# Kernel optimization log

Hardware: AMD Instinct MI355X
Metric: run time of the kernel (lower is better)

The kernel has to match this reference:

```python
import jax, jax.numpy as jnp
import numpy as np

ALPHA = 0.25
GAMMA = 2.0
EPS = 1e-4


def calc_iou(a, b):
    # a: [A,4] anchors xyxy, b: [M,4] gt boxes xyxy -> [A,M]
    area = (b[:, 2] - b[:, 0]) * (b[:, 3] - b[:, 1])  # [M]
    iw = jnp.minimum(a[:, 2:3], b[None, :, 2]) - jnp.maximum(a[:, 0:1], b[None, :, 0])
    ih = jnp.minimum(a[:, 3:4], b[None, :, 3]) - jnp.maximum(a[:, 1:2], b[None, :, 1])
    iw = jnp.clip(iw, 0.0)
    ih = jnp.clip(ih, 0.0)
    anchor_area = ((a[:, 2] - a[:, 0]) * (a[:, 3] - a[:, 1]))[:, None]
    ua = jnp.clip(anchor_area + area[None, :] - iw * ih, 1e-8)
    return iw * ih / ua


def setup_inputs() -> dict:
    B, A, K, M = 8, 120000, 80, 32
    key = jax.random.key(0)
    k1, k2, k3, k4, k5, k6, k7 = jax.random.split(key, 7)
    classifications = jax.random.uniform(k1, (B, A, K), dtype=jnp.float32)
    regressions = jax.random.normal(k2, (B, A, 4), dtype=jnp.float32) * 0.1
    # anchors: valid xyxy boxes with positive width/height
    a_xy = jax.random.uniform(k3, (A, 2), minval=0.0, maxval=480.0)
    a_wh = jax.random.uniform(k4, (A, 2), minval=16.0, maxval=128.0)
    anchors = jnp.concatenate([a_xy, a_xy + a_wh], axis=1)[None].astype(jnp.float32)
    # annotations: [B, M, 5] valid gt boxes, labels in [0, K)
    g_xy = jax.random.uniform(k5, (B, M, 2), minval=0.0, maxval=400.0)
    g_wh = jax.random.uniform(k6, (B, M, 2), minval=20.0, maxval=120.0)
    labels = jax.random.randint(k7, (B, M, 1), 0, K).astype(jnp.float32)
    annotations = jnp.concatenate([g_xy, g_xy + g_wh, labels], axis=2).astype(jnp.float32)
    return {"classifications": classifications, "regressions": regressions,
            "anchors": anchors, "annotations": annotations}


def reference(classifications, regressions, anchors, annotations):
    anchor = anchors[0]  # [A,4]
    aw = anchor[:, 2] - anchor[:, 0]
    ah = anchor[:, 3] - anchor[:, 1]
    acx = anchor[:, 0] + 0.5 * aw
    acy = anchor[:, 1] + 0.5 * ah
    reg_scale = jnp.array([0.1, 0.1, 0.2, 0.2], dtype=classifications.dtype)

    def per_item(cls, reg, ann):
        # cls: [A,K], reg: [A,4], ann: [M,5]
        valid = ann[:, 4] != -1.0  # [M] padding mask
        c = jnp.clip(cls, EPS, 1.0 - EPS)
        iou = jnp.where(valid[None, :], calc_iou(anchor, ann[:, :4]), -1.0)  # [A,M]
        iou_max = iou.max(axis=1)
        iou_argmax = iou.argmax(axis=1)
        assigned = ann[iou_argmax]  # [A,5] gather
        pos = iou_max >= 0.5
        neg = iou_max < 0.4
        num_pos = pos.sum().astype(c.dtype)
        # targets: 1 at assigned class for positives, 0 for negatives, -1 = ignore
        onehot = jax.nn.one_hot(assigned[:, 4].astype(jnp.int32), c.shape[1], dtype=c.dtype)
        t = jnp.where(pos[:, None], onehot, jnp.where(neg[:, None], 0.0, -1.0))
        alpha_factor = jnp.where(t == 1.0, ALPHA, 1.0 - ALPHA)
        focal_weight = jnp.where(t == 1.0, 1.0 - c, c)
        bce = -(t * jnp.log(c) + (1.0 - t) * jnp.log(1.0 - c))
        cls_loss = jnp.where(t != -1.0, alpha_factor * focal_weight ** GAMMA * bce, 0.0)
        cls_loss = cls_loss.sum() / jnp.maximum(num_pos, 1.0)
        gw0 = assigned[:, 2] - assigned[:, 0]
        gh0 = assigned[:, 3] - assigned[:, 1]
        gcx = assigned[:, 0] + 0.5 * gw0
        gcy = assigned[:, 1] + 0.5 * gh0
        gw = jnp.maximum(gw0, 1.0)
        gh = jnp.maximum(gh0, 1.0)
        rt = jnp.stack([(gcx - acx) / aw, (gcy - acy) / ah,
                        jnp.log(gw / aw), jnp.log(gh / ah)], axis=1) / reg_scale
        diff = jnp.abs(rt - reg)
        smooth = jnp.where(diff <= 1.0 / 9.0, 0.5 * 9.0 * diff ** 2, diff - 0.5 / 9.0)
        reg_loss = jnp.where(num_pos > 0.0,
                             (smooth * pos[:, None]).sum() / jnp.maximum(num_pos * 4.0, 1.0),
                             0.0)
        return cls_loss, reg_loss

    cls_l, reg_l = jax.vmap(per_item)(classifications, regressions, annotations)
    return cls_l.mean(keepdims=True), reg_l.mean(keepdims=True)
```

## Files before the change

kernel.cpp:

```cpp
#include <hip/hip_runtime.h>

#define NB 8
#define NA 120000
#define NK 80
#define NM 32

#define ALPHA_F 0.25f
#define EPS_F 1e-4f

#define TPB (NA / 64)
#define BLKW 4
#define BPBW ((TPB + BLKW - 1) / BLKW)


typedef float f32x4 __attribute__((ext_vector_type(4)));

__device__ __forceinline__ f32x4 ntload4(const f32x4* p) {
    return __builtin_nontemporal_load(p);
}

__device__ __forceinline__ float clampc(float x) {
    return fminf(fmaxf(x, EPS_F), 1.0f - EPS_F);
}
__device__ __forceinline__ float negl(float c) {
    return (1.0f - ALPHA_F) * c * c * (-__logf(1.0f - c));
}
__device__ __forceinline__ float posl(float c) {
    const float omc = 1.0f - c;
    return ALPHA_F * omc * omc * (-__logf(c));
}
__device__ __forceinline__ float negl4v(f32x4 v) {
    return negl(clampc(v.x)) + negl(clampc(v.y)) + negl(clampc(v.z)) + negl(clampc(v.w));
}

__global__ __launch_bounds__(256) void fused_kernel(
    const float* __restrict__ anchors,
    const float* __restrict__ regressions,
    const float* __restrict__ annotations,
    const float* __restrict__ cls,
    float* __restrict__ part)
{
    const int b = blockIdx.x / BPBW;
    const int blk = blockIdx.x % BPBW;
    const int wid = threadIdx.x >> 6;
    const int lane = threadIdx.x & 63;
    const int tile = blk * BLKW + wid;

    __shared__ float ann[NM * 5];
    __shared__ float barea[NM];
    if (threadIdx.x < NM * 5) ann[threadIdx.x] = annotations[b * NM * 5 + threadIdx.x];
    __syncthreads();
    if (threadIdx.x < NM) {
        const float* r = &ann[threadIdx.x * 5];
        barea[threadIdx.x] = (r[2] - r[0]) * (r[3] - r[1]);
    }
    __syncthreads();

    float reg_local = 0.0f;
    float pos_local = 0.0f;
    float cls_local = 0.0f;

    if (tile < TPB) {
        const int a = tile * 64 + lane;
        float maskf = 1.0f;

        {
            const float4 av = ((const float4*)anchors)[a];
            const float aw = av.z - av.x;
            const float ah = av.w - av.y;
            const float aarea = aw * ah;

            float bi = -1.0f, bu = 1.0f;
            int bm = 0;
            #pragma unroll
            for (int m = 0; m < NM; ++m) {
                const float bx1 = ann[m * 5 + 0];
                const float by1 = ann[m * 5 + 1];
                const float bx2 = ann[m * 5 + 2];
                const float by2 = ann[m * 5 + 3];
                const float lbl = ann[m * 5 + 4];
                const float iw = fmaxf(fminf(av.z, bx2) - fmaxf(av.x, bx1), 0.0f);
                const float ih = fmaxf(fminf(av.w, by2) - fmaxf(av.y, by1), 0.0f);
                float inter = iw * ih;
                float ua = fmaxf(aarea + barea[m] - inter, 1e-8f);
                if (lbl == -1.0f) { inter = -1.0f; ua = 1.0f; }
                if (m == 0 || inter * bu > bi * ua) { bi = inter; bu = ua; bm = m; }
            }

            if (bi >= 0.5f * bu) {
                const int st = (int)ann[bm * 5 + 4];
                const float bx1 = ann[bm * 5 + 0];
                const float by1 = ann[bm * 5 + 1];
                const float bx2 = ann[bm * 5 + 2];
                const float by2 = ann[bm * 5 + 3];
                const float gw0 = bx2 - bx1;
                const float gh0 = by2 - by1;
                const float gcx = bx1 + 0.5f * gw0;
                const float gcy = by1 + 0.5f * gh0;
                const float gw = fmaxf(gw0, 1.0f);
                const float gh = fmaxf(gh0, 1.0f);
                const float acx = av.x + 0.5f * aw;
                const float acy = av.y + 0.5f * ah;
                const float rt0 = ((gcx - acx) / aw) / 0.1f;
                const float rt1 = ((gcy - acy) / ah) / 0.1f;
                const float rt2 = logf(gw / aw) / 0.2f;
                const float rt3 = logf(gh / ah) / 0.2f;
                const float4 rg = ((const float4*)regressions)[b * NA + a];
                float s = 0.0f, d;
                d = fabsf(rt0 - rg.x); s += (d <= 1.0f / 9.0f) ? 4.5f * d * d : d - 0.5f / 9.0f;
                d = fabsf(rt1 - rg.y); s += (d <= 1.0f / 9.0f) ? 4.5f * d * d : d - 0.5f / 9.0f;
                d = fabsf(rt2 - rg.z); s += (d <= 1.0f / 9.0f) ? 4.5f * d * d : d - 0.5f / 9.0f;
                d = fabsf(rt3 - rg.w); s += (d <= 1.0f / 9.0f) ? 4.5f * d * d : d - 0.5f / 9.0f;
                reg_local = s;
                pos_local = 1.0f;
                const float c = clampc(cls[((size_t)b * NA + a) * NK + st]);
                cls_local = posl(c) - negl(c);
            } else if (bi >= 0.4f * bu) {
                maskf = 0.0f;
            }
        }

        const f32x4* __restrict__ p =
            (const f32x4*)(cls + ((size_t)b * NA + (size_t)tile * 64) * NK);
        float sum = 0.0f;
        #pragma unroll
        for (int o = 0; o < 4; ++o) {
            f32x4 v[5];
            #pragma unroll
            for (int u = 0; u < 5; ++u)
                v[u] = ntload4(p + (o * 5 + u) * 64 + lane);
            #pragma unroll
            for (int u = 0; u < 5; ++u) {
                const int flat = (o * 5 + u) * 64 + lane;
                const int row = flat / 20;
                const float m = __shfl(maskf, row, 64);
                sum += m * negl4v(v[u]);
            }
        }
        cls_local += sum;
    }

    #pragma unroll
    for (int o = 32; o > 0; o >>= 1) {
        cls_local += __shfl_down(cls_local, o, 64);
        reg_local += __shfl_down(reg_local, o, 64);
        pos_local += __shfl_down(pos_local, o, 64);
    }
    __shared__ float wc[BLKW], wr[BLKW], wp[BLKW];
    if (lane == 0) { wc[wid] = cls_local; wr[wid] = reg_local; wp[wid] = pos_local; }
    __syncthreads();
    if (threadIdx.x == 0) {
        float csum = 0.0f, rsum = 0.0f, psum = 0.0f;
        #pragma unroll
        for (int i = 0; i < BLKW; ++i) { csum += wc[i]; rsum += wr[i]; psum += wp[i]; }
        float4 o4;
        o4.x = csum; o4.y = rsum; o4.z = psum; o4.w = 0.0f;
        ((float4*)part)[blockIdx.x] = o4;
    }
}

__global__ __launch_bounds__(512) void finalize_kernel(
    const float* __restrict__ part,
    float* __restrict__ out)
{
    __shared__ float redC[NB], redR[NB], redP[NB];
    const int w = threadIdx.x >> 6;
    const int lane = threadIdx.x & 63;

    float c = 0.0f, r = 0.0f, p = 0.0f;
    #pragma unroll
    for (int u = 0; u < 8; ++u) {
        const int i = u * 64 + lane;
        if (i < BPBW) {
            const float4 q = ((const float4*)part)[w * BPBW + i];
            c += q.x; r += q.y; p += q.z;
        }
    }
    #pragma unroll
    for (int o = 32; o > 0; o >>= 1) {
        c += __shfl_down(c, o, 64);
        r += __shfl_down(r, o, 64);
        p += __shfl_down(p, o, 64);
    }
    if (lane == 0) { redC[w] = c; redR[w] = r; redP[w] = p; }
    __syncthreads();
    if (threadIdx.x == 0) {
        float cs = 0.0f, rs = 0.0f;
        #pragma unroll
        for (int b = 0; b < NB; ++b) {
            const float P = redP[b];
            cs += redC[b] / fmaxf(P, 1.0f);
            rs += (P > 0.0f) ? redR[b] / fmaxf(P * 4.0f, 1.0f) : 0.0f;
        }
        out[0] = cs / (float)NB;
        out[1] = rs / (float)NB;
    }
}

extern "C" void kernel_launch(void* const* d_in, const int* in_sizes, int n_in,
                              void* d_out, int out_size, void* d_ws, size_t ws_size,
                              hipStream_t stream) {
    const float* cls = (const float*)d_in[0];
    const float* reg = (const float*)d_in[1];
    const float* anc = (const float*)d_in[2];
    const float* ann = (const float*)d_in[3];

    float* part = (float*)d_ws;
    float* out = (float*)d_out;

    fused_kernel<<<NB * BPBW, 256, 0, stream>>>(anc, reg, ann, cls, part);
    finalize_kernel<<<1, 512, 0, stream>>>(part, out);
}
```

Baseline: 76.66 us.

## Split fused loss kernel into streaming negative-loss and positive-assignment kernels

The single fused kernel is split in two. A streaming kernel computes only the IoU mask and the negative focal loss over the classification tensor, and a separate assign kernel recomputes IoU to handle the positive anchors' regression and class correction. The aim is to take the divergent positive-anchor branch and its registers out of the bandwidth-bound stream, which gets launch bounds of 8 blocks per SM for higher occupancy. The cost is a second launch that redoes the 32-box IoU scan and an extra partials buffer that the finalize kernel must read.

New measurement: 148.4 us. +93.6%, slower.

```diff
diff --git a/kernel.cpp b/kernel.cpp
--- a/kernel.cpp
+++ b/kernel.cpp
@@ -12,6 +12,7 @@
 #define BLKW 4
 #define BPBW ((TPB + BLKW - 1) / BLKW)
 
+#define PART_A_OFF 16384
 
 typedef float f32x4 __attribute__((ext_vector_type(4)));
 
@@ -33,12 +34,11 @@
     return negl(clampc(v.x)) + negl(clampc(v.y)) + negl(clampc(v.z)) + negl(clampc(v.w));
 }
 
-__global__ __launch_bounds__(256) void fused_kernel(
+__global__ __launch_bounds__(256, 8) void stream_kernel(
     const float* __restrict__ anchors,
-    const float* __restrict__ regressions,
     const float* __restrict__ annotations,
     const float* __restrict__ cls,
-    float* __restrict__ part)
+    float* __restrict__ part_s)
 {
     const int b = blockIdx.x / BPBW;
     const int blk = blockIdx.x % BPBW;
@@ -56,9 +56,7 @@
     }
     __syncthreads();
 
-    float reg_local = 0.0f;
-    float pos_local = 0.0f;
-    float cls_local = 0.0f;
+    float sum = 0.0f;
 
     if (tile < TPB) {
         const int a = tile * 64 + lane;
@@ -66,12 +64,8 @@
 
         {
             const float4 av = ((const float4*)anchors)[a];
-            const float aw = av.z - av.x;
-            const float ah = av.w - av.y;
-            const float aarea = aw * ah;
-
+            const float aarea = (av.z - av.x) * (av.w - av.y);
             float bi = -1.0f, bu = 1.0f;
-            int bm = 0;
             #pragma unroll
             for (int m = 0; m < NM; ++m) {
                 const float bx1 = ann[m * 5 + 0];
@@ -84,45 +78,13 @@
                 float inter = iw * ih;
                 float ua = fmaxf(aarea + barea[m] - inter, 1e-8f);
                 if (lbl == -1.0f) { inter = -1.0f; ua = 1.0f; }
-                if (m == 0 || inter * bu > bi * ua) { bi = inter; bu = ua; bm = m; }
+                if (m == 0 || inter * bu > bi * ua) { bi = inter; bu = ua; }
             }
-
-            if (bi >= 0.5f * bu) {
-                const int st = (int)ann[bm * 5 + 4];
-                const float bx1 = ann[bm * 5 + 0];
-                const float by1 = ann[bm * 5 + 1];
-                const float bx2 = ann[bm * 5 + 2];
-                const float by2 = ann[bm * 5 + 3];
-                const float gw0 = bx2 - bx1;
-                const float gh0 = by2 - by1;
-                const float gcx = bx1 + 0.5f * gw0;
-                const float gcy = by1 + 0.5f * gh0;
-                const float gw = fmaxf(gw0, 1.0f);
-                const float gh = fmaxf(gh0, 1.0f);
-                const float acx = av.x + 0.5f * aw;
-                const float acy = av.y + 0.5f * ah;
-                const float rt0 = ((gcx - acx) / aw) / 0.1f;
-                const float rt1 = ((gcy - acy) / ah) / 0.1f;
-                const float rt2 = logf(gw / aw) / 0.2f;
-                const float rt3 = logf(gh / ah) / 0.2f;
-                const float4 rg = ((const float4*)regressions)[b * NA + a];
-                float s = 0.0f, d;
-                d = fabsf(rt0 - rg.x); s += (d <= 1.0f / 9.0f) ? 4.5f * d * d : d - 0.5f / 9.0f;
-                d = fabsf(rt1 - rg.y); s += (d <= 1.0f / 9.0f) ? 4.5f * d * d : d - 0.5f / 9.0f;
-                d = fabsf(rt2 - rg.z); s += (d <= 1.0f / 9.0f) ? 4.5f * d * d : d - 0.5f / 9.0f;
-                d = fabsf(rt3 - rg.w); s += (d <= 1.0f / 9.0f) ? 4.5f * d * d : d - 0.5f / 9.0f;
-                reg_local = s;
-                pos_local = 1.0f;
-                const float c = clampc(cls[((size_t)b * NA + a) * NK + st]);
-                cls_local = posl(c) - negl(c);
-            } else if (bi >= 0.4f * bu) {
-                maskf = 0.0f;
-            }
+            if (bi >= 0.4f * bu && bi < 0.5f * bu) maskf = 0.0f;
         }
 
         const f32x4* __restrict__ p =
             (const f32x4*)(cls + ((size_t)b * NA + (size_t)tile * 64) * NK);
-        float sum = 0.0f;
         #pragma unroll
         for (int o = 0; o < 4; ++o) {
             f32x4 v[5];
@@ -137,7 +99,101 @@
                 sum += m * negl4v(v[u]);
             }
         }
-        cls_local += sum;
+    }
+
+    #pragma unroll
+    for (int o = 32; o > 0; o >>= 1) sum += __shfl_down(sum, o, 64);
+    __shared__ float ws[BLKW];
+    if (lane == 0) ws[wid] = sum;
+    __syncthreads();
+    if (threadIdx.x == 0) {
+        float s = 0.0f;
+        #pragma unroll
+        for (int i = 0; i < BLKW; ++i) s += ws[i];
+        part_s[blockIdx.x] = s;
+    }
+}
+
+__global__ __launch_bounds__(256) void assign_kernel(
+    const float* __restrict__ anchors,
+    const float* __restrict__ regressions,
+    const float* __restrict__ annotations,
+    const float* __restrict__ cls,
+    float* __restrict__ part_a)
+{
+    const int b = blockIdx.x / BPBW;
+    const int blk = blockIdx.x % BPBW;
+    const int wid = threadIdx.x >> 6;
+    const int lane = threadIdx.x & 63;
+    const int tile = blk * BLKW + wid;
+
+    __shared__ float ann[NM * 5];
+    __shared__ float barea[NM];
+    if (threadIdx.x < NM * 5) ann[threadIdx.x] = annotations[b * NM * 5 + threadIdx.x];
+    __syncthreads();
+    if (threadIdx.x < NM) {
+        const float* r = &ann[threadIdx.x * 5];
+        barea[threadIdx.x] = (r[2] - r[0]) * (r[3] - r[1]);
+    }
+    __syncthreads();
+
+    float reg_local = 0.0f;
+    float pos_local = 0.0f;
+    float cls_local = 0.0f;
+
+    if (tile < TPB) {
+        const int a = tile * 64 + lane;
+        const float4 av = ((const float4*)anchors)[a];
+        const float aw = av.z - av.x;
+        const float ah = av.w - av.y;
+        const float aarea = aw * ah;
+
+        float bi = -1.0f, bu = 1.0f;
+        int bm = 0;
+        #pragma unroll
+        for (int m = 0; m < NM; ++m) {
+            const float bx1 = ann[m * 5 + 0];
+            const float by1 = ann[m * 5 + 1];
+            const float bx2 = ann[m * 5 + 2];
+            const float by2 = ann[m * 5 + 3];
+            const float lbl = ann[m * 5 + 4];
+            const float iw = fmaxf(fminf(av.z, bx2) - fmaxf(av.x, bx1), 0.0f);
+            const float ih = fmaxf(fminf(av.w, by2) - fmaxf(av.y, by1), 0.0f);
+            float inter = iw * ih;
+            float ua = fmaxf(aarea + barea[m] - inter, 1e-8f);
+            if (lbl == -1.0f) { inter = -1.0f; ua = 1.0f; }
+            if (m == 0 || inter * bu > bi * ua) { bi = inter; bu = ua; bm = m; }
+        }
+
+        if (bi >= 0.5f * bu) {
+            const int st = (int)ann[bm * 5 + 4];
+            const float bx1 = ann[bm * 5 + 0];
+            const float by1 = ann[bm * 5 + 1];
+            const float bx2 = ann[bm * 5 + 2];
+            const float by2 = ann[bm * 5 + 3];
+            const float gw0 = bx2 - bx1;
+            const float gh0 = by2 - by1;
+            const float gcx = bx1 + 0.5f * gw0;
+            const float gcy = by1 + 0.5f * gh0;
+            const float gw = fmaxf(gw0, 1.0f);
+            const float gh = fmaxf(gh0, 1.0f);
+            const float acx = av.x + 0.5f * aw;
+            const float acy = av.y + 0.5f * ah;
+            const float rt0 = ((gcx - acx) / aw) / 0.1f;
+            const float rt1 = ((gcy - acy) / ah) / 0.1f;
+            const float rt2 = logf(gw / aw) / 0.2f;
+            const float rt3 = logf(gh / ah) / 0.2f;
+            const float4 rg = ((const float4*)regressions)[b * NA + a];
+            float s = 0.0f, d;
+            d = fabsf(rt0 - rg.x); s += (d <= 1.0f / 9.0f) ? 4.5f * d * d : d - 0.5f / 9.0f;
+            d = fabsf(rt1 - rg.y); s += (d <= 1.0f / 9.0f) ? 4.5f * d * d : d - 0.5f / 9.0f;
+            d = fabsf(rt2 - rg.z); s += (d <= 1.0f / 9.0f) ? 4.5f * d * d : d - 0.5f / 9.0f;
+            d = fabsf(rt3 - rg.w); s += (d <= 1.0f / 9.0f) ? 4.5f * d * d : d - 0.5f / 9.0f;
+            reg_local = s;
+            pos_local = 1.0f;
+            const float c = clampc(cls[((size_t)b * NA + a) * NK + st]);
+            cls_local = posl(c) - negl(c);
+        }
     }
 
     #pragma unroll
@@ -155,12 +211,13 @@
         for (int i = 0; i < BLKW; ++i) { csum += wc[i]; rsum += wr[i]; psum += wp[i]; }
         float4 o4;
         o4.x = csum; o4.y = rsum; o4.z = psum; o4.w = 0.0f;
-        ((float4*)part)[blockIdx.x] = o4;
+        ((float4*)part_a)[blockIdx.x] = o4;
     }
 }
 
 __global__ __launch_bounds__(512) void finalize_kernel(
-    const float* __restrict__ part,
+    const float* __restrict__ part_s,
+    const float* __restrict__ part_a,
     float* __restrict__ out)
 {
     __shared__ float redC[NB], redR[NB], redP[NB];
@@ -172,7 +229,8 @@
     for (int u = 0; u < 8; ++u) {
         const int i = u * 64 + lane;
         if (i < BPBW) {
-            const float4 q = ((const float4*)part)[w * BPBW + i];
+            c += part_s[w * BPBW + i];
+            const float4 q = ((const float4*)part_a)[w * BPBW + i];
             c += q.x; r += q.y; p += q.z;
         }
     }
@@ -205,9 +263,11 @@
     const float* anc = (const float*)d_in[2];
     const float* ann = (const float*)d_in[3];
 
-    float* part = (float*)d_ws;
+    float* part_s = (float*)d_ws;
+    float* part_a = (float*)((char*)d_ws + PART_A_OFF);
     float* out = (float*)d_out;
 
-    fused_kernel<<<NB * BPBW, 256, 0, stream>>>(anc, reg, ann, cls, part);
-    finalize_kernel<<<1, 512, 0, stream>>>(part, out);
-}
+    stream_kernel<<<NB * BPBW, 256, 0, stream>>>(anc, ann, cls, part_s);
+    assign_kernel<<<NB * BPBW, 256, 0, stream>>>(anc, reg, ann, cls, part_a);
+    finalize_kernel<<<1, 512, 0, stream>>>(part_s, part_a, out);
+}
```
